# Optimization experiments

Hardware: AMD Instinct MI355X
Metric: run time of the kernel (lower is better)

## Reference

```python
import jax, jax.numpy as jnp
import numpy as np


def setup_inputs() -> dict:
    key = jax.random.key(0)
    k1, k2, k3, k4 = jax.random.split(key, 4)
    B, C_in, C_out, H, W = 8, 256, 256, 160, 160
    mask = jax.random.randint(k1, (B, 1, H, W), 0, 2, dtype=jnp.int32)  # binary hard mask
    ori = jax.random.normal(k2, (B, C_in, H, W), dtype=jnp.float32)
    weight = jax.random.normal(k3, (C_out, C_in, 3, 3), dtype=jnp.float32) * 0.02
    bias = jax.random.normal(k4, (C_out,), dtype=jnp.float32) * 0.02
    return {"mask": mask, "ori": ori, "weight": weight, "bias": bias}


def reference(mask, ori, weight, bias):
    # apply_mask: broadcast binary [B,1,H,W] mask over channels, zero masked regions
    x = ori * mask.astype(ori.dtype)
    # dense 3x3 conv, stride 1, padding 1 (SAME) -> output [B, C_out, H, W]
    out = jax.lax.conv_general_dilated(
        x, weight,
        window_strides=(1, 1),
        padding='SAME',
        dimension_numbers=('NCHW', 'OIHW', 'NCHW'),
    )
    return out + bias[None, :, None, None]
```

## Files before the change

### kernel.cpp

```cpp
#include <hip/hip_runtime.h>

typedef __attribute__((ext_vector_type(8))) short short8;
typedef __attribute__((ext_vector_type(4))) float f32x4;

#define B_    8
#define CI    256
#define CO    256
#define Hh    160
#define Ww    160
#define HP    162
#define WP    162
#define HWp   (Hh * Ww)
#define XPAD_ELEMS (B_ * HP * WP * CI)
#define W2_ELEMS   (9 * CI * CO)
#define NT    36

__device__ __forceinline__ unsigned short f2bf(float f) {
  unsigned int u = __float_as_uint(f);
  u += 0x7FFFu + ((u >> 16) & 1u);
  return (unsigned short)(u >> 16);
}

__global__ void prep_w_kernel(const float* __restrict__ w, unsigned short* __restrict__ w2) {
  int i = blockIdx.x * 256 + threadIdx.x;
  if (i >= W2_ELEMS) return;
  int ci = i & 255;
  int t = i >> 8;
  int co = t & 255;
  int s = t >> 8;
  w2[i] = f2bf(w[(co * 256 + ci) * 9 + s]);
}

__global__ void zero_border(unsigned short* __restrict__ xp) {
  int g = blockIdx.x * 256 + threadIdx.x;
  int pos = g >> 5;
  int c = (g & 31) << 3;
  int n = pos / 644;
  int p = pos - n * 644;
  int y, x;
  if (p < 324) { y = (p < 162) ? 0 : 161; x = (p < 162) ? p : p - 162; }
  else { int q = p - 324; y = 1 + (q >> 1); x = (q & 1) ? 161 : 0; }
  unsigned short* d = xp + (((size_t)(n * 162 + y)) * 162 + x) * 256 + c;
  *(uint4*)d = (uint4){0u, 0u, 0u, 0u};
}

__global__ void prep_x_kernel(const float* __restrict__ ori, const int* __restrict__ mask,
                              unsigned short* __restrict__ xp) {
  int bid = blockIdx.x;
  int wt = bid % 3;
  int t1 = bid / 3;
  int cit = t1 & 3;
  int t2 = t1 >> 2;
  int h = t2 % Hh;
  int n = t2 / Hh;
  int t = threadIdx.x;

  __shared__ float tile[64][65];

  int wl = t & 63;
  int w = wt * 64 + wl;
  bool valid = (w < Ww);
  float m = 0.f;
  if (valid) m = (float)mask[(n * Hh + h) * Ww + w];
  const float* src = ori + (((size_t)(n * CI + cit * 64) * Hh + h) * Ww + w);
  int r0 = t >> 6;
#pragma unroll
  for (int k = 0; k < 16; ++k) {
    int ci_l = r0 * 16 + k;
    float v = 0.f;
    if (valid) v = src[(size_t)ci_l * HWp] * m;
    tile[ci_l][wl] = v;
  }
  __syncthreads();

  int wl2 = t >> 2;
  int wo = wt * 64 + wl2;
  if (wo < Ww) {
    int cseg = (t & 3) * 16;
    union { unsigned short u[8]; uint4 v; } p0, p1;
#pragma unroll
    for (int j = 0; j < 8; ++j) p0.u[j] = f2bf(tile[cseg + j][wl2]);
#pragma unroll
    for (int j = 0; j < 8; ++j) p1.u[j] = f2bf(tile[cseg + 8 + j][wl2]);
    unsigned short* dst = xp + ((size_t)((n * HP + h + 1) * WP) + (wo + 1)) * CI + cit * 64 + cseg;
    *(uint4*)dst = p0.v;
    *(uint4*)(dst + 8) = p1.v;
  }
}

__device__ __forceinline__ void gload16(const unsigned short* g, unsigned short* l) {
  __builtin_amdgcn_global_load_lds((const __attribute__((address_space(1))) void*)g,
                                   (__attribute__((address_space(3))) void*)l, 16, 0, 0);
}

__global__ void __launch_bounds__(512, 2) sconv_gemm(const unsigned short* __restrict__ xp,
                                                     const unsigned short* __restrict__ w2,
                                                     const float* __restrict__ bias,
                                                     float* __restrict__ out) {
  __shared__ unsigned short lds[2][26624];

  const int bid = blockIdx.x;
  const int n = bid & 7;
  const int h = bid >> 3;

  const int t = threadIdx.x;
  const int l = t & 63;
  const int wv = t >> 6;
  const int wm = wv & 3;
  const int wn = wv >> 2;

  const int lr = l >> 3;
  const int lane_stage = (wv * 8 + lr) * 256 + (((l & 7) ^ lr) << 3);
  const unsigned xrow_base = (unsigned)(n * HP + h) * WP;

  const int lc = l & 15;
  const int cs0 = (((l >> 4)) ^ (l & 7)) << 3;
  const int cs1 = ((4 + (l >> 4)) ^ (l & 7)) << 3;

  f32x4 acc[4][5];
#pragma unroll
  for (int mi = 0; mi < 4; ++mi)
#pragma unroll
    for (int ni = 0; ni < 5; ++ni)
      acc[mi][ni] = (f32x4){0.f, 0.f, 0.f, 0.f};

  auto STAGE = [&](int tt) {
    int shift = tt >> 2;
    int kh = shift / 3;
    int kw = shift - kh * 3;
    int ci0 = (tt & 3) << 6;
    const unsigned short* ag = w2 + shift * (CI * CO) + ci0 + lane_stage;
    const unsigned short* bg = xp + ((size_t)(xrow_base + kh * WP + kw) << 8) + ci0 + lane_stage;
    unsigned short* sa = &lds[tt & 1][0];
    unsigned short* sb = &lds[tt & 1][16384];
#pragma unroll
    for (int r = 0; r < 4; ++r)
      gload16(ag + r * 16384, sa + (r * 64 + wv * 8) * 64);
#pragma unroll
    for (int r = 0; r < 2; ++r)
      gload16(bg + r * 16384, sb + (r * 64 + wv * 8) * 64);
    if (wv < 4)
      gload16(bg + 32768, sb + (128 + wv * 8) * 64);
  };

  STAGE(0);
  STAGE(1);
  asm volatile("s_waitcnt vmcnt(6)" ::: "memory");
  __builtin_amdgcn_s_barrier();

  for (int tt = 0; tt < NT; ++tt) {
    const unsigned short* Ab = &lds[tt & 1][0];
    const unsigned short* Bb = &lds[tt & 1][16384];

    short8 bf[5][2];
#pragma unroll
    for (int ni = 0; ni < 5; ++ni) {
      const unsigned short* br = Bb + (wn * 80 + ni * 16 + lc) * 64;
      bf[ni][0] = *(const short8*)(br + cs0);
      bf[ni][1] = *(const short8*)(br + cs1);
    }
#pragma unroll
    for (int mi = 0; mi < 4; ++mi) {
      const unsigned short* ar = Ab + (wm * 64 + mi * 16 + lc) * 64;
      short8 a0 = *(const short8*)(ar + cs0);
      short8 a1 = *(const short8*)(ar + cs1);
      __builtin_amdgcn_s_setprio(1);
#pragma unroll
      for (int ni = 0; ni < 5; ++ni) {
        acc[mi][ni] = __builtin_amdgcn_mfma_f32_16x16x32_bf16(a0, bf[ni][0], acc[mi][ni], 0, 0, 0);
        acc[mi][ni] = __builtin_amdgcn_mfma_f32_16x16x32_bf16(a1, bf[ni][1], acc[mi][ni], 0, 0, 0);
      }
      __builtin_amdgcn_s_setprio(0);
    }

    __syncthreads();
    if (tt + 2 < NT) STAGE(tt + 2);
  }

  const int co_l = (l >> 4) * 4;
#pragma unroll
  for (int mi = 0; mi < 4; ++mi) {
    int cobase = wm * 64 + mi * 16 + co_l;
    const float4 bv = *(const float4*)(bias + cobase);
    size_t obase = ((size_t)n * CO + cobase) * HWp + (size_t)h * Ww;
#pragma unroll
    for (int ni = 0; ni < 5; ++ni) {
      int w = wn * 80 + ni * 16 + lc;
      f32x4 v = acc[mi][ni];
      out[obase + w]             = v[0] + bv.x;
      out[obase + HWp + w]       = v[1] + bv.y;
      out[obase + 2 * HWp + w]   = v[2] + bv.z;
      out[obase + 3 * HWp + w]   = v[3] + bv.w;
    }
  }
}

extern "C" void kernel_launch(void* const* d_in, const int* in_sizes, int n_in,
                              void* d_out, int out_size, void* d_ws, size_t ws_size,
                              hipStream_t stream) {
  const int* mask = (const int*)d_in[0];
  const float* ori = (const float*)d_in[1];
  const float* weight = (const float*)d_in[2];
  const float* bias = (const float*)d_in[3];
  float* out = (float*)d_out;

  unsigned short* xp = (unsigned short*)d_ws;
  unsigned short* w2 = xp + XPAD_ELEMS;

  zero_border<<<644, 256, 0, stream>>>(xp);
  prep_w_kernel<<<(W2_ELEMS + 255) / 256, 256, 0, stream>>>(weight, w2);
  prep_x_kernel<<<B_ * Hh * 4 * 3, 256, 0, stream>>>(ori, mask, xp);
  sconv_gemm<<<B_ * Hh, 512, 0, stream>>>(xp, w2, bias, out);
}
```

Baseline: 343.5 us.

## Retile conv GEMM to 128-pixel blocks with 32x32 MFMA and register-loaded weights

Restructures the implicit-GEMM conv so each 256-thread block computes all 256 output channels for 128 flattened pixels, not one image row. Only the activations are staged in LDS. Weights are pre-packed into an MFMA-fragment layout and loaded straight from global/L2 into registers. The inner product switches from 16x16x32 to 32x32x16 bf16 MFMA, and blocks are remapped across XCDs. This cuts LDS traffic and instruction count, at the cost of per-iteration global weight loads that may stall without LDS prefetch, plus a more scattered output store pattern.

```diff
diff --git a/kernel.cpp b/kernel.cpp
--- a/kernel.cpp
+++ b/kernel.cpp
@@ -1,7 +1,7 @@
 #include <hip/hip_runtime.h>
 
 typedef __attribute__((ext_vector_type(8))) short short8;
-typedef __attribute__((ext_vector_type(4))) float f32x4;
+typedef __attribute__((ext_vector_type(16))) float f32x16;
 
 #define B_    8
 #define CI    256
@@ -12,8 +12,10 @@
 #define WP    162
 #define HWp   (Hh * Ww)
 #define XPAD_ELEMS (B_ * HP * WP * CI)
-#define W2_ELEMS   (9 * CI * CO)
+#define W3_ELEMS   (9 * CI * CO)
 #define NT    36
+#define BPX   128
+#define NBLK  1600
 
 __device__ __forceinline__ unsigned short f2bf(float f) {
   unsigned int u = __float_as_uint(f);
@@ -21,14 +23,19 @@
   return (unsigned short)(u >> 16);
 }
 
-__global__ void prep_w_kernel(const float* __restrict__ w, unsigned short* __restrict__ w2) {
+__global__ void prep_w_kernel(const float* __restrict__ w, unsigned short* __restrict__ w3) {
   int i = blockIdx.x * 256 + threadIdx.x;
-  if (i >= W2_ELEMS) return;
-  int ci = i & 255;
-  int t = i >> 8;
-  int co = t & 255;
-  int s = t >> 8;
-  w2[i] = f2bf(w[(co * 256 + ci) * 9 + s]);
+  if (i >= W3_ELEMS) return;
+  int e = i & 7;
+  int l = (i >> 3) & 63;
+  int s = (i >> 9) & 3;
+  int mt = (i >> 11) & 7;
+  int tt = i >> 14;
+  int shift = tt >> 2;
+  int cic = tt & 3;
+  int co = mt * 32 + (l & 31);
+  int ci = cic * 64 + s * 16 + (l >> 5) * 8 + e;
+  w3[i] = f2bf(w[(co * 256 + ci) * 9 + shift]);
 }
 
 __global__ void zero_border(unsigned short* __restrict__ xp) {
@@ -93,83 +100,80 @@
                                    (__attribute__((address_space(3))) void*)l, 16, 0, 0);
 }
 
-__global__ void __launch_bounds__(512, 2) sconv_gemm(const unsigned short* __restrict__ xp,
-                                                     const unsigned short* __restrict__ w2,
+__global__ void __launch_bounds__(256, 2) sconv_gemm(const unsigned short* __restrict__ xp,
+                                                     const unsigned short* __restrict__ w3,
                                                      const float* __restrict__ bias,
                                                      float* __restrict__ out) {
-  __shared__ unsigned short lds[2][26624];
-
-  const int bid = blockIdx.x;
-  const int n = bid & 7;
-  const int h = bid >> 3;
+  __shared__ unsigned short Bs[2][BPX * 64];
+
+  int braw = blockIdx.x;
+  int bid = (braw & 7) * (NBLK / 8) + (braw >> 3);
+  const int p0 = bid * BPX;
 
   const int t = threadIdx.x;
   const int l = t & 63;
   const int wv = t >> 6;
-  const int wm = wv & 3;
-  const int wn = wv >> 2;
-
-  const int lr = l >> 3;
-  const int lane_stage = (wv * 8 + lr) * 256 + (((l & 7) ^ lr) << 3);
-  const unsigned xrow_base = (unsigned)(n * HP + h) * WP;
-
-  const int lc = l & 15;
-  const int cs0 = (((l >> 4)) ^ (l & 7)) << 3;
-  const int cs1 = ((4 + (l >> 4)) ^ (l & 7)) << 3;
-
-  f32x4 acc[4][5];
-#pragma unroll
-  for (int mi = 0; mi < 4; ++mi)
-#pragma unroll
-    for (int ni = 0; ni < 5; ++ni)
-      acc[mi][ni] = (f32x4){0.f, 0.f, 0.f, 0.f};
+
+  unsigned boff[4];
+#pragma unroll
+  for (int rr = 0; rr < 4; ++rr) {
+    int pxl = wv * 32 + rr * 8 + (l >> 3);
+    int p = p0 + pxl;
+    int n = p / HWp;
+    int hw = p - n * HWp;
+    int h = hw / Ww;
+    int w = hw - h * Ww;
+    boff[rr] = (unsigned)((n * HP + h) * WP + w) * CI + (((l & 7) ^ (l >> 3)) << 3);
+  }
+
+  const int brow = (l & 31) * 64;
+  const int bx = l & 7;
+  const int bhi = l >> 5;
+
+  f32x16 acc[2][4];
+#pragma unroll
+  for (int mi = 0; mi < 2; ++mi)
+#pragma unroll
+    for (int ni = 0; ni < 4; ++ni)
+      acc[mi][ni] = (f32x16)(0.f);
 
   auto STAGE = [&](int tt) {
     int shift = tt >> 2;
     int kh = shift / 3;
     int kw = shift - kh * 3;
-    int ci0 = (tt & 3) << 6;
-    const unsigned short* ag = w2 + shift * (CI * CO) + ci0 + lane_stage;
-    const unsigned short* bg = xp + ((size_t)(xrow_base + kh * WP + kw) << 8) + ci0 + lane_stage;
-    unsigned short* sa = &lds[tt & 1][0];
-    unsigned short* sb = &lds[tt & 1][16384];
-#pragma unroll
-    for (int r = 0; r < 4; ++r)
-      gload16(ag + r * 16384, sa + (r * 64 + wv * 8) * 64);
-#pragma unroll
-    for (int r = 0; r < 2; ++r)
-      gload16(bg + r * 16384, sb + (r * 64 + wv * 8) * 64);
-    if (wv < 4)
-      gload16(bg + 32768, sb + (128 + wv * 8) * 64);
+    unsigned bd = (unsigned)(kh * WP + kw) * CI + ((tt & 3) << 6);
+    unsigned short* sb = &Bs[tt & 1][(wv * 32) * 64];
+#pragma unroll
+    for (int rr = 0; rr < 4; ++rr)
+      gload16(xp + boff[rr] + bd, sb + rr * 512);
   };
 
   STAGE(0);
   STAGE(1);
-  asm volatile("s_waitcnt vmcnt(6)" ::: "memory");
+  asm volatile("s_waitcnt vmcnt(4)" ::: "memory");
   __builtin_amdgcn_s_barrier();
 
   for (int tt = 0; tt < NT; ++tt) {
-    const unsigned short* Ab = &lds[tt & 1][0];
-    const unsigned short* Bb = &lds[tt & 1][16384];
-
-    short8 bf[5][2];
-#pragma unroll
-    for (int ni = 0; ni < 5; ++ni) {
-      const unsigned short* br = Bb + (wn * 80 + ni * 16 + lc) * 64;
-      bf[ni][0] = *(const short8*)(br + cs0);
-      bf[ni][1] = *(const short8*)(br + cs1);
-    }
-#pragma unroll
-    for (int mi = 0; mi < 4; ++mi) {
-      const unsigned short* ar = Ab + (wm * 64 + mi * 16 + lc) * 64;
-      short8 a0 = *(const short8*)(ar + cs0);
-      short8 a1 = *(const short8*)(ar + cs1);
+    short8 a[2][4];
+#pragma unroll
+    for (int mi = 0; mi < 2; ++mi)
+#pragma unroll
+      for (int s = 0; s < 4; ++s)
+        a[mi][s] = *(const short8*)(w3 + ((size_t)(((tt * 8 + (wv * 2 + mi)) * 4 + s) * 64 + l) << 3));
+
+    const unsigned short* Bb = Bs[tt & 1];
+#pragma unroll
+    for (int s = 0; s < 4; ++s) {
+      short8 bf[4];
+#pragma unroll
+      for (int ni = 0; ni < 4; ++ni)
+        bf[ni] = *(const short8*)(Bb + ni * 2048 + brow + ((((s << 1) + bhi) ^ bx) << 3));
       __builtin_amdgcn_s_setprio(1);
 #pragma unroll
-      for (int ni = 0; ni < 5; ++ni) {
-        acc[mi][ni] = __builtin_amdgcn_mfma_f32_16x16x32_bf16(a0, bf[ni][0], acc[mi][ni], 0, 0, 0);
-        acc[mi][ni] = __builtin_amdgcn_mfma_f32_16x16x32_bf16(a1, bf[ni][1], acc[mi][ni], 0, 0, 0);
-      }
+      for (int mi = 0; mi < 2; ++mi)
+#pragma unroll
+        for (int ni = 0; ni < 4; ++ni)
+          acc[mi][ni] = __builtin_amdgcn_mfma_f32_32x32x16_bf16(a[mi][s], bf[ni], acc[mi][ni], 0, 0, 0);
       __builtin_amdgcn_s_setprio(0);
     }
 
@@ -177,20 +181,31 @@
     if (tt + 2 < NT) STAGE(tt + 2);
   }
 
-  const int co_l = (l >> 4) * 4;
-#pragma unroll
-  for (int mi = 0; mi < 4; ++mi) {
-    int cobase = wm * 64 + mi * 16 + co_l;
-    const float4 bv = *(const float4*)(bias + cobase);
-    size_t obase = ((size_t)n * CO + cobase) * HWp + (size_t)h * Ww;
-#pragma unroll
-    for (int ni = 0; ni < 5; ++ni) {
-      int w = wn * 80 + ni * 16 + lc;
-      f32x4 v = acc[mi][ni];
-      out[obase + w]             = v[0] + bv.x;
-      out[obase + HWp + w]       = v[1] + bv.y;
-      out[obase + 2 * HWp + w]   = v[2] + bv.z;
-      out[obase + 3 * HWp + w]   = v[3] + bv.w;
+  float4 bv[2][4];
+#pragma unroll
+  for (int mi = 0; mi < 2; ++mi)
+#pragma unroll
+    for (int g = 0; g < 4; ++g)
+      bv[mi][g] = *(const float4*)(bias + wv * 64 + mi * 32 + g * 8 + 4 * bhi);
+
+#pragma unroll
+  for (int ni = 0; ni < 4; ++ni) {
+    int p = p0 + ni * 32 + (l & 31);
+    int n = p / HWp;
+    int hw = p - n * HWp;
+    float* op = out + (size_t)n * (CO * HWp) + hw;
+#pragma unroll
+    for (int mi = 0; mi < 2; ++mi) {
+      int cob = wv * 64 + mi * 32 + 4 * bhi;
+#pragma unroll
+      for (int g = 0; g < 4; ++g) {
+#pragma unroll
+        for (int r = 0; r < 4; ++r) {
+          int q = g * 4 + r;
+          int co = cob + r + 8 * g;
+          op[(size_t)co * HWp] = acc[mi][ni][q] + ((const float*)&bv[mi][g])[r];
+        }
+      }
     }
   }
 }
@@ -205,10 +220,10 @@
   float* out = (float*)d_out;
 
   unsigned short* xp = (unsigned short*)d_ws;
-  unsigned short* w2 = xp + XPAD_ELEMS;
+  unsigned short* w3 = xp + XPAD_ELEMS;
 
   zero_border<<<644, 256, 0, stream>>>(xp);
-  prep_w_kernel<<<(W2_ELEMS + 255) / 256, 256, 0, stream>>>(weight, w2);
+  prep_w_kernel<<<(W3_ELEMS + 255) / 256, 256, 0, stream>>>(weight, w3);
   prep_x_kernel<<<B_ * Hh * 4 * 3, 256, 0, stream>>>(ori, mask, xp);
-  sconv_gemm<<<B_ * Hh, 512, 0, stream>>>(xp, w2, bias, out);
-}
+  sconv_gemm<<<NBLK, 256, 0, stream>>>(xp, w3, bias, out);
+}
```

Result: slower. 387.9 us (+12.9%).

## Retile conv GEMM to 128x256 blocks with 32x32 MFMA and triple buffering

Applied to the files above, without the earlier changes.

Each block in the implicit-GEMM conv now covers a 128 output-channel by 256 flattened-pixel tile, replacing the old one-row, all-channels tile, and uses 32x32x16 bf16 MFMAs with 2x2 accumulators per wave. The K loop runs input-channel chunks on the outside and filter taps on the inside. LDS goes to three buffers so the next stage can be issued before compute, with a single waitcnt and barrier per iteration. The aim is better operand reuse per LDS read and fewer synchronizations. In exchange, occupancy drops to one block per CU and the launch grows to 1600 blocks, each holding more accumulator registers.

```diff
diff --git a/kernel.cpp b/kernel.cpp
--- a/kernel.cpp
+++ b/kernel.cpp
@@ -1,7 +1,7 @@
 #include <hip/hip_runtime.h>
 
 typedef __attribute__((ext_vector_type(8))) short short8;
-typedef __attribute__((ext_vector_type(4))) float f32x4;
+typedef __attribute__((ext_vector_type(16))) float f32x16;
 
 #define B_    8
 #define CI    256
@@ -14,6 +14,8 @@
 #define XPAD_ELEMS (B_ * HP * WP * CI)
 #define W2_ELEMS   (9 * CI * CO)
 #define NT    36
+#define ASZ   (128 * 64)
+#define SLOT  (ASZ + 256 * 64)
 
 __device__ __forceinline__ unsigned short f2bf(float f) {
   unsigned int u = __float_as_uint(f);
@@ -93,54 +95,62 @@
                                    (__attribute__((address_space(3))) void*)l, 16, 0, 0);
 }
 
-__global__ void __launch_bounds__(512, 2) sconv_gemm(const unsigned short* __restrict__ xp,
+__global__ void __launch_bounds__(512, 1) sconv_gemm(const unsigned short* __restrict__ xp,
                                                      const unsigned short* __restrict__ w2,
                                                      const float* __restrict__ bias,
                                                      float* __restrict__ out) {
-  __shared__ unsigned short lds[2][26624];
-
-  const int bid = blockIdx.x;
-  const int n = bid & 7;
-  const int h = bid >> 3;
+  __shared__ unsigned short lds[3 * SLOT];
+
+  int raw = blockIdx.x;
+  int n = raw & 7;
+  int seq = raw >> 3;
+  int cot = seq & 1;
+  int pxt = seq >> 1;
+  const int co0 = cot * 128;
+  const int hw0 = pxt * 256;
 
   const int t = threadIdx.x;
   const int l = t & 63;
   const int wv = t >> 6;
-  const int wm = wv & 3;
-  const int wn = wv >> 2;
+  const int wm = wv >> 2;
+  const int wn = wv & 3;
 
   const int lr = l >> 3;
-  const int lane_stage = (wv * 8 + lr) * 256 + (((l & 7) ^ lr) << 3);
-  const unsigned xrow_base = (unsigned)(n * HP + h) * WP;
-
-  const int lc = l & 15;
-  const int cs0 = (((l >> 4)) ^ (l & 7)) << 3;
-  const int cs1 = ((4 + (l >> 4)) ^ (l & 7)) << 3;
-
-  f32x4 acc[4][5];
-#pragma unroll
-  for (int mi = 0; mi < 4; ++mi)
-#pragma unroll
-    for (int ni = 0; ni < 5; ++ni)
-      acc[mi][ni] = (f32x4){0.f, 0.f, 0.f, 0.f};
+  const int swz8 = ((l & 7) ^ lr) << 3;
+  unsigned aoff[2];
+#pragma unroll
+  for (int g = 0; g < 2; ++g)
+    aoff[g] = (unsigned)(co0 + wv * 16 + g * 8 + lr) * 256 + swz8;
+  unsigned boff[4];
+#pragma unroll
+  for (int g = 0; g < 4; ++g) {
+    int hw = hw0 + wv * 32 + g * 8 + lr;
+    int h = hw / Ww;
+    int w = hw - h * Ww;
+    boff[g] = (unsigned)((n * HP + h) * WP + w) * 256 + swz8;
+  }
+
+  f32x16 acc[2][2];
+#pragma unroll
+  for (int mi = 0; mi < 2; ++mi)
+#pragma unroll
+    for (int ni = 0; ni < 2; ++ni)
+      acc[mi][ni] = (f32x16)(0.f);
 
   auto STAGE = [&](int tt) {
-    int shift = tt >> 2;
-    int kh = shift / 3;
+    int cic = (tt * 57) >> 9;
+    int shift = tt - cic * 9;
+    int kh = (shift * 11) >> 5;
     int kw = shift - kh * 3;
-    int ci0 = (tt & 3) << 6;
-    const unsigned short* ag = w2 + shift * (CI * CO) + ci0 + lane_stage;
-    const unsigned short* bg = xp + ((size_t)(xrow_base + kh * WP + kw) << 8) + ci0 + lane_stage;
-    unsigned short* sa = &lds[tt & 1][0];
-    unsigned short* sb = &lds[tt & 1][16384];
-#pragma unroll
-    for (int r = 0; r < 4; ++r)
-      gload16(ag + r * 16384, sa + (r * 64 + wv * 8) * 64);
-#pragma unroll
-    for (int r = 0; r < 2; ++r)
-      gload16(bg + r * 16384, sb + (r * 64 + wv * 8) * 64);
-    if (wv < 4)
-      gload16(bg + 32768, sb + (128 + wv * 8) * 64);
+    unsigned ad = (unsigned)shift * (CI * CO) + (cic << 6);
+    unsigned bd = (unsigned)(kh * WP + kw) * 256 + (cic << 6);
+    unsigned short* s = &lds[(tt % 3) * SLOT];
+#pragma unroll
+    for (int g = 0; g < 2; ++g)
+      gload16(w2 + ad + aoff[g], s + (wv * 16 + g * 8) * 64);
+#pragma unroll
+    for (int g = 0; g < 4; ++g)
+      gload16(xp + bd + boff[g], s + ASZ + (wv * 32 + g * 8) * 64);
   };
 
   STAGE(0);
@@ -148,49 +158,56 @@
   asm volatile("s_waitcnt vmcnt(6)" ::: "memory");
   __builtin_amdgcn_s_barrier();
 
+  const int l31 = l & 31;
+  const int bhi = l >> 5;
+  const int lx = l & 7;
+
   for (int tt = 0; tt < NT; ++tt) {
-    const unsigned short* Ab = &lds[tt & 1][0];
-    const unsigned short* Bb = &lds[tt & 1][16384];
-
-    short8 bf[5][2];
-#pragma unroll
-    for (int ni = 0; ni < 5; ++ni) {
-      const unsigned short* br = Bb + (wn * 80 + ni * 16 + lc) * 64;
-      bf[ni][0] = *(const short8*)(br + cs0);
-      bf[ni][1] = *(const short8*)(br + cs1);
-    }
-#pragma unroll
-    for (int mi = 0; mi < 4; ++mi) {
-      const unsigned short* ar = Ab + (wm * 64 + mi * 16 + lc) * 64;
-      short8 a0 = *(const short8*)(ar + cs0);
-      short8 a1 = *(const short8*)(ar + cs1);
+    if (tt + 2 < NT) STAGE(tt + 2);
+
+    const unsigned short* A = &lds[(tt % 3) * SLOT];
+    const unsigned short* Bb = A + ASZ;
+    const unsigned short* ar = A + (wm * 64 + l31) * 64;
+    const unsigned short* br = Bb + (wn * 64 + l31) * 64;
+
+#pragma unroll
+    for (int s = 0; s < 4; ++s) {
+      int so = (((s << 1) + bhi) ^ lx) << 3;
+      short8 a0 = *(const short8*)(ar + so);
+      short8 a1 = *(const short8*)(ar + 32 * 64 + so);
+      short8 b0 = *(const short8*)(br + so);
+      short8 b1 = *(const short8*)(br + 32 * 64 + so);
       __builtin_amdgcn_s_setprio(1);
-#pragma unroll
-      for (int ni = 0; ni < 5; ++ni) {
-        acc[mi][ni] = __builtin_amdgcn_mfma_f32_16x16x32_bf16(a0, bf[ni][0], acc[mi][ni], 0, 0, 0);
-        acc[mi][ni] = __builtin_amdgcn_mfma_f32_16x16x32_bf16(a1, bf[ni][1], acc[mi][ni], 0, 0, 0);
-      }
+      acc[0][0] = __builtin_amdgcn_mfma_f32_32x32x16_bf16(a0, b0, acc[0][0], 0, 0, 0);
+      acc[0][1] = __builtin_amdgcn_mfma_f32_32x32x16_bf16(a0, b1, acc[0][1], 0, 0, 0);
+      acc[1][0] = __builtin_amdgcn_mfma_f32_32x32x16_bf16(a1, b0, acc[1][0], 0, 0, 0);
+      acc[1][1] = __builtin_amdgcn_mfma_f32_32x32x16_bf16(a1, b1, acc[1][1], 0, 0, 0);
       __builtin_amdgcn_s_setprio(0);
     }
 
-    __syncthreads();
-    if (tt + 2 < NT) STAGE(tt + 2);
-  }
-
-  const int co_l = (l >> 4) * 4;
-#pragma unroll
-  for (int mi = 0; mi < 4; ++mi) {
-    int cobase = wm * 64 + mi * 16 + co_l;
-    const float4 bv = *(const float4*)(bias + cobase);
-    size_t obase = ((size_t)n * CO + cobase) * HWp + (size_t)h * Ww;
-#pragma unroll
-    for (int ni = 0; ni < 5; ++ni) {
-      int w = wn * 80 + ni * 16 + lc;
-      f32x4 v = acc[mi][ni];
-      out[obase + w]             = v[0] + bv.x;
-      out[obase + HWp + w]       = v[1] + bv.y;
-      out[obase + 2 * HWp + w]   = v[2] + bv.z;
-      out[obase + 3 * HWp + w]   = v[3] + bv.w;
+    if (tt == 34)
+      asm volatile("s_waitcnt vmcnt(0) lgkmcnt(0)" ::: "memory");
+    else
+      asm volatile("s_waitcnt vmcnt(6) lgkmcnt(0)" ::: "memory");
+    __builtin_amdgcn_s_barrier();
+  }
+
+#pragma unroll
+  for (int mi = 0; mi < 2; ++mi) {
+    int cobase = co0 + wm * 64 + mi * 32 + 4 * bhi;
+#pragma unroll
+    for (int ni = 0; ni < 2; ++ni) {
+      int px = hw0 + wn * 64 + ni * 32 + l31;
+      float* op = out + ((size_t)n * CO) * HWp + px;
+      f32x16 v = acc[mi][ni];
+#pragma unroll
+      for (int g = 0; g < 4; ++g) {
+        int co = cobase + 8 * g;
+        const float4 bv = *(const float4*)(bias + co);
+#pragma unroll
+        for (int r = 0; r < 4; ++r)
+          op[(size_t)(co + r) * HWp] = v[g * 4 + r] + ((const float*)&bv)[r];
+      }
     }
   }
 }
@@ -210,5 +227,5 @@
   zero_border<<<644, 256, 0, stream>>>(xp);
   prep_w_kernel<<<(W2_ELEMS + 255) / 256, 256, 0, stream>>>(weight, w2);
   prep_x_kernel<<<B_ * Hh * 4 * 3, 256, 0, stream>>>(ori, mask, xp);
-  sconv_gemm<<<B_ * Hh, 512, 0, stream>>>(xp, w2, bias, out);
-}
+  sconv_gemm<<<1600, 512, 0, stream>>>(xp, w2, bias, out);
+}
```

Result: slower. 395.5 us (+15.1%).

## Stage padded input strip once per channel chunk and reuse across all 9 taps

Applied to the files above, without the earlier changes.

Each block now computes 4 output rows by 128 output channels instead of 1 row by 256 channels. It loads a 6-row padded input strip per 64-channel chunk into LDS once and reuses it for all 9 kernel shifts, streaming only weight tiles per tap. This cuts redundant global and LDS traffic for the im2col B operand. The cost is higher register use (4x10 accumulators), occupancy dropping to 1 block per CU, and a full vmcnt(0) wait plus barrier every step, which serialises load and compute with less overlap.

```diff
diff --git a/kernel.cpp b/kernel.cpp
--- a/kernel.cpp
+++ b/kernel.cpp
@@ -13,7 +13,8 @@
 #define HWp   (Hh * Ww)
 #define XPAD_ELEMS (B_ * HP * WP * CI)
 #define W2_ELEMS   (9 * CI * CO)
-#define NT    36
+#define SOFF  16384
+#define SROW  (168 * 64)
 
 __device__ __forceinline__ unsigned short f2bf(float f) {
   unsigned int u = __float_as_uint(f);
@@ -93,104 +94,127 @@
                                    (__attribute__((address_space(3))) void*)l, 16, 0, 0);
 }
 
-__global__ void __launch_bounds__(512, 2) sconv_gemm(const unsigned short* __restrict__ xp,
+__global__ void __launch_bounds__(512, 1) sconv_gemm(const unsigned short* __restrict__ xp,
                                                      const unsigned short* __restrict__ w2,
                                                      const float* __restrict__ bias,
                                                      float* __restrict__ out) {
-  __shared__ unsigned short lds[2][26624];
+  __shared__ unsigned short lds[SOFF + 6 * SROW];
 
   const int bid = blockIdx.x;
   const int n = bid & 7;
-  const int h = bid >> 3;
+  const int rest = bid >> 3;
+  const int cot = rest & 1;
+  const int rg = rest >> 1;
+  const int r0 = rg * 4;
+  const int co0 = cot * 128;
+  const unsigned h0p = (unsigned)(n * HP + r0);
 
   const int t = threadIdx.x;
   const int l = t & 63;
   const int wv = t >> 6;
-  const int wm = wv & 3;
-  const int wn = wv >> 2;
+  const int wm = wv & 1;
+  const int wn = wv >> 1;
 
   const int lr = l >> 3;
-  const int lane_stage = (wv * 8 + lr) * 256 + (((l & 7) ^ lr) << 3);
-  const unsigned xrow_base = (unsigned)(n * HP + h) * WP;
-
+  const int swz8 = ((l & 7) ^ lr) << 3;
   const int lc = l & 15;
-  const int cs0 = (((l >> 4)) ^ (l & 7)) << 3;
-  const int cs1 = ((4 + (l >> 4)) ^ (l & 7)) << 3;
-
-  f32x4 acc[4][5];
+  const int hi4 = l >> 4;
+  const int lx = l & 7;
+
+  const unsigned arow0 = (unsigned)(co0 + wv * 16 + lr) * 256 + swz8;
+  const int acu = (wm * 64 + lc) * 64;
+  const int bub = wn * SROW + lc * 64;
+
+  f32x4 acc[4][10];
 #pragma unroll
   for (int mi = 0; mi < 4; ++mi)
 #pragma unroll
-    for (int ni = 0; ni < 5; ++ni)
+    for (int ni = 0; ni < 10; ++ni)
       acc[mi][ni] = (f32x4){0.f, 0.f, 0.f, 0.f};
 
-  auto STAGE = [&](int tt) {
-    int shift = tt >> 2;
-    int kh = shift / 3;
-    int kw = shift - kh * 3;
-    int ci0 = (tt & 3) << 6;
-    const unsigned short* ag = w2 + shift * (CI * CO) + ci0 + lane_stage;
-    const unsigned short* bg = xp + ((size_t)(xrow_base + kh * WP + kw) << 8) + ci0 + lane_stage;
-    unsigned short* sa = &lds[tt & 1][0];
-    unsigned short* sb = &lds[tt & 1][16384];
-#pragma unroll
-    for (int r = 0; r < 4; ++r)
-      gload16(ag + r * 16384, sa + (r * 64 + wv * 8) * 64);
-#pragma unroll
-    for (int r = 0; r < 2; ++r)
-      gload16(bg + r * 16384, sb + (r * 64 + wv * 8) * 64);
-    if (wv < 4)
-      gload16(bg + 32768, sb + (128 + wv * 8) * 64);
+  auto STAGE_A = [&](int slot, int shift, int cic) {
+    const unsigned short* src = w2 + shift * 65536 + (cic << 6) + arow0;
+    unsigned short* dst = lds + slot * 8192 + (wv * 16) * 64;
+    gload16(src, dst);
+    gload16(src + 2048, dst + 512);
   };
 
-  STAGE(0);
-  STAGE(1);
-  asm volatile("s_waitcnt vmcnt(6)" ::: "memory");
+  auto STAGE_STRIP = [&](int cic) {
+#pragma unroll
+    for (int k = 0; k < 16; ++k) {
+      int g = wv + 8 * k;
+      if (g < 126) {
+        int khr = g / 21;
+        int gg = g - khr * 21;
+        const unsigned short* src = xp + ((size_t)(h0p + khr) * WP + gg * 8 + lr) * 256
+                                       + (cic << 6) + swz8;
+        gload16(src, lds + SOFF + khr * SROW + (gg * 8) * 64);
+      }
+    }
+  };
+
+  STAGE_STRIP(0);
+  STAGE_A(0, 0, 0);
+  asm volatile("s_waitcnt vmcnt(0)" ::: "memory");
   __builtin_amdgcn_s_barrier();
 
-  for (int tt = 0; tt < NT; ++tt) {
-    const unsigned short* Ab = &lds[tt & 1][0];
-    const unsigned short* Bb = &lds[tt & 1][16384];
-
-    short8 bf[5][2];
-#pragma unroll
-    for (int ni = 0; ni < 5; ++ni) {
-      const unsigned short* br = Bb + (wn * 80 + ni * 16 + lc) * 64;
-      bf[ni][0] = *(const short8*)(br + cs0);
-      bf[ni][1] = *(const short8*)(br + cs1);
+  for (int cic = 0; cic < 4; ++cic) {
+    for (int s = 0; s < 9; ++s) {
+      const int tt = cic * 9 + s;
+      if (s < 8) STAGE_A((tt + 1) & 1, s + 1, cic);
+      else if (cic < 3) STAGE_A((tt + 1) & 1, 0, cic + 1);
+
+      const int kh = (s >= 6) ? 2 : (s >= 3 ? 1 : 0);
+      const int kw = s - kh * 3;
+      const unsigned short* As = lds + (tt & 1) * 8192;
+      const int koff = SOFF + bub + (kh * 168 + kw) * 64;
+      const int xb = (lc + kw) & 7;
+
+#pragma unroll
+      for (int kk = 0; kk < 2; ++kk) {
+        const int sa = (((kk << 2) + hi4) ^ lx) << 3;
+        const int sb = (((kk << 2) + hi4) ^ xb) << 3;
+        short8 a[4];
+#pragma unroll
+        for (int mi = 0; mi < 4; ++mi)
+          a[mi] = *(const short8*)(As + acu + mi * 1024 + sa);
+#pragma unroll
+        for (int ni = 0; ni < 10; ++ni) {
+          short8 b = *(const short8*)(lds + koff + ni * 1024 + sb);
+          __builtin_amdgcn_s_setprio(1);
+#pragma unroll
+          for (int mi = 0; mi < 4; ++mi)
+            acc[mi][ni] = __builtin_amdgcn_mfma_f32_16x16x32_bf16(a[mi], b, acc[mi][ni], 0, 0, 0);
+          __builtin_amdgcn_s_setprio(0);
+        }
+      }
+
+      if (s == 8 && cic < 3) {
+        __builtin_amdgcn_s_barrier();
+        STAGE_STRIP(cic + 1);
+        asm volatile("s_waitcnt vmcnt(0)" ::: "memory");
+        __builtin_amdgcn_s_barrier();
+      } else {
+        asm volatile("s_waitcnt vmcnt(0)" ::: "memory");
+        __builtin_amdgcn_s_barrier();
+      }
     }
-#pragma unroll
-    for (int mi = 0; mi < 4; ++mi) {
-      const unsigned short* ar = Ab + (wm * 64 + mi * 16 + lc) * 64;
-      short8 a0 = *(const short8*)(ar + cs0);
-      short8 a1 = *(const short8*)(ar + cs1);
-      __builtin_amdgcn_s_setprio(1);
-#pragma unroll
-      for (int ni = 0; ni < 5; ++ni) {
-        acc[mi][ni] = __builtin_amdgcn_mfma_f32_16x16x32_bf16(a0, bf[ni][0], acc[mi][ni], 0, 0, 0);
-        acc[mi][ni] = __builtin_amdgcn_mfma_f32_16x16x32_bf16(a1, bf[ni][1], acc[mi][ni], 0, 0, 0);
-      }
-      __builtin_amdgcn_s_setprio(0);
-    }
-
-    __syncthreads();
-    if (tt + 2 < NT) STAGE(tt + 2);
-  }
-
-  const int co_l = (l >> 4) * 4;
+  }
+
+  const int orow = r0 + wn;
 #pragma unroll
   for (int mi = 0; mi < 4; ++mi) {
-    int cobase = wm * 64 + mi * 16 + co_l;
+    int cobase = co0 + wm * 64 + mi * 16 + hi4 * 4;
     const float4 bv = *(const float4*)(bias + cobase);
-    size_t obase = ((size_t)n * CO + cobase) * HWp + (size_t)h * Ww;
-#pragma unroll
-    for (int ni = 0; ni < 5; ++ni) {
-      int w = wn * 80 + ni * 16 + lc;
+    float* op = out + (((size_t)n * CO + cobase) * Hh + orow) * Ww;
+#pragma unroll
+    for (int ni = 0; ni < 10; ++ni) {
+      int w = ni * 16 + lc;
       f32x4 v = acc[mi][ni];
-      out[obase + w]             = v[0] + bv.x;
-      out[obase + HWp + w]       = v[1] + bv.y;
-      out[obase + 2 * HWp + w]   = v[2] + bv.z;
-      out[obase + 3 * HWp + w]   = v[3] + bv.w;
+      op[w]               = v[0] + bv.x;
+      op[(size_t)Hh * Ww + w]     = v[1] + bv.y;
+      op[(size_t)2 * Hh * Ww + w] = v[2] + bv.z;
+      op[(size_t)3 * Hh * Ww + w] = v[3] + bv.w;
     }
   }
 }
@@ -210,5 +234,5 @@
   zero_border<<<644, 256, 0, stream>>>(xp);
   prep_w_kernel<<<(W2_ELEMS + 255) / 256, 256, 0, stream>>>(weight, w2);
   prep_x_kernel<<<B_ * Hh * 4 * 3, 256, 0, stream>>>(ori, mask, xp);
-  sconv_gemm<<<B_ * Hh, 512, 0, stream>>>(xp, w2, bias, out);
-}
+  sconv_gemm<<<640, 512, 0, stream>>>(xp, w2, bias, out);
+}
```

Result: slower. 361.0 us (+5.1%).
